# Kernel tuning notes

Measured on AMD Instinct MI355X. Metric: run time of the kernel, lower is better.

The kernel has to match this reference:

```python
import jax, jax.numpy as jnp
import numpy as np

NUM_CLASSES = 60
FEATURE_DIM = 256
SEQ_LEN = 128
NUM_HEADS = 8
TOP_M = 20  # min(20, seq_len)
NUM_LAYERS = 2
EPS = 1e-5


def _layernorm(x, g, b):
    m = x.mean(-1, keepdims=True)
    v = ((x - m) ** 2).mean(-1, keepdims=True)
    return (x - m) * jax.lax.rsqrt(v + EPS) * g + b


def _topm_attention(x, qkv_w, qkv_b, proj_w, proj_b):
    # x: (B, N, C). Weights stored as (in, out) so y = x @ W + b.
    B, N, C = x.shape
    hd = C // NUM_HEADS
    scale = hd ** -0.5
    qkv = (x @ qkv_w + qkv_b).reshape(B, N, 3, NUM_HEADS, hd)
    q, k, v = (jnp.moveaxis(qkv[:, :, i], 2, 1) for i in range(3))  # (B,H,N,hd)
    s = jnp.einsum('bhnd,bhmd->bhnm', q, k) * scale  # (B,H,N,N)
    if TOP_M < N:
        # keep only per-query top-m scores (threshold at the m-th largest;
        # identical to torch scatter-mask for distinct float scores)
        kth = jax.lax.top_k(s, TOP_M)[0][..., -1:]
        s = jnp.where(s >= kth, s, -jnp.inf)
    a = jax.nn.softmax(s, axis=-1)  # dropout is identity in eval
    o = jnp.einsum('bhnm,bhmd->bhnd', a, v)
    o = o.transpose(0, 2, 1, 3).reshape(B, N, C)
    return o @ proj_w + proj_b


def setup_inputs() -> dict:
    key = jax.random.key(0)
    ks = jax.random.split(key, 20)
    B = 8 * NUM_CLASSES
    C = FEATURE_DIM
    d = {
        'reweighted_features': jax.random.normal(ks[0], (B, C, SEQ_LEN), jnp.float32),
        'pos_embed': jax.random.normal(ks[1], (1, SEQ_LEN, C), jnp.float32) * 0.02,
        'cls_w1': jax.random.normal(ks[2], (C, C // 2), jnp.float32) / np.sqrt(C),
        'cls_b1': jnp.zeros((C // 2,), jnp.float32),
        'cls_w2': jax.random.normal(ks[3], (C // 2, 1), jnp.float32) / np.sqrt(C // 2),
        'cls_b2': jnp.zeros((1,), jnp.float32),
    }
    for i in range(NUM_LAYERS):
        d[f'qkv_w{i}'] = jax.random.normal(ks[4 + 4 * i], (C, 3 * C), jnp.float32) / np.sqrt(C)
        d[f'qkv_b{i}'] = jnp.zeros((3 * C,), jnp.float32)
        d[f'proj_w{i}'] = jax.random.normal(ks[5 + 4 * i], (C, C), jnp.float32) / np.sqrt(C)
        d[f'proj_b{i}'] = jnp.zeros((C,), jnp.float32)
        d[f'ln_g{i}'] = jnp.ones((C,), jnp.float32)
        d[f'ln_b{i}'] = jnp.zeros((C,), jnp.float32)
    return d


def reference(reweighted_features, pos_embed, cls_w1, cls_b1, cls_w2, cls_b2,
              qkv_w0, qkv_b0, proj_w0, proj_b0, ln_g0, ln_b0,
              qkv_w1, qkv_b1, proj_w1, proj_b1, ln_g1, ln_b1):
    B = reweighted_features.shape[0] // NUM_CLASSES
    x = reweighted_features.transpose(0, 2, 1)  # (B*cls, N, C)
    x = x + pos_embed
    layers = [(qkv_w0, qkv_b0, proj_w0, proj_b0, ln_g0, ln_b0),
              (qkv_w1, qkv_b1, proj_w1, proj_b1, ln_g1, ln_b1)]
    for qw, qb, pw, pb, g, b in layers:
        x = _layernorm(x + _topm_attention(x, qw, qb, pw, pb), g, b)
    x = x.mean(axis=1)  # (B*cls, C)
    x = x.reshape(B, NUM_CLASSES, FEATURE_DIM)
    h = jax.nn.relu(x @ cls_w1 + cls_b1)  # dropout identity in eval
    logits = (h @ cls_w2 + cls_b2).reshape(B, NUM_CLASSES)
    return logits
```

## Files before the change

### kernel.cpp

```cpp
#include <hip/hip_runtime.h>
#include <hip/hip_bf16.h>
#include <cmath>

#define NSEQ 480
#define SEQN 128
#define CDIM 256
#define NH 8
#define HD 32
#define TOPM 20

typedef float f32x4 __attribute__((ext_vector_type(4)));
typedef short bf16x8 __attribute__((ext_vector_type(8)));

__device__ __forceinline__ unsigned short bf16_rn(float x) {
    unsigned int u = __float_as_uint(x);
    unsigned int r = (u + 0x7FFFu + ((u >> 16) & 1u)) >> 16;
    return (unsigned short)r;
}
__device__ __forceinline__ float bf16f(unsigned short h) {
    return __uint_as_float(((unsigned int)h) << 16);
}
__device__ __forceinline__ unsigned int okey(float v) {
    unsigned int u = __float_as_uint(v);
    return (u >> 31) ? ~u : (u | 0x80000000u);
}
__device__ __forceinline__ float okey_inv(unsigned int k) {
    return __uint_as_float((k >> 31) ? (k & 0x7FFFFFFFu) : ~k);
}
__device__ __forceinline__ unsigned pk_bf16(float a, float b) {
    union { __hip_bfloat162 h; unsigned u; } cv;
    cv.h = __float22bfloat162_rn(make_float2(a, b));
    return cv.u;
}
__device__ __forceinline__ void unpack_bf16x8(uint4 u, float* o) {
    o[0] = bf16f((unsigned short)(u.x & 0xffffu)); o[1] = bf16f((unsigned short)(u.x >> 16));
    o[2] = bf16f((unsigned short)(u.y & 0xffffu)); o[3] = bf16f((unsigned short)(u.y >> 16));
    o[4] = bf16f((unsigned short)(u.z & 0xffffu)); o[5] = bf16f((unsigned short)(u.z >> 16));
    o[6] = bf16f((unsigned short)(u.w & 0xffffu)); o[7] = bf16f((unsigned short)(u.w >> 16));
}

__global__ __launch_bounds__(256) void prep_kernel(const float* __restrict__ RW,
                                                   const float* __restrict__ POS,
                                                   unsigned short* __restrict__ XH,
                                                   unsigned short* __restrict__ XL) {
    int b = blockIdx.x, n0 = blockIdx.y * 32, c0 = blockIdx.z * 32;
    __shared__ float tile[32][33];
    int tx = threadIdx.x & 31, ty = threadIdx.x >> 5;
#pragma unroll
    for (int jj = 0; jj < 4; ++jj) {
        int c = c0 + ty + 8 * jj;
        tile[ty + 8 * jj][tx] = RW[((size_t)b * CDIM + c) * SEQN + n0 + tx];
    }
    __syncthreads();
#pragma unroll
    for (int jj = 0; jj < 4; ++jj) {
        int n = n0 + ty + 8 * jj;
        int c = c0 + tx;
        float val = tile[tx][ty + 8 * jj] + POS[n * CDIM + c];
        unsigned short hi = bf16_rn(val);
        size_t idx = (size_t)b * SEQN * CDIM + n * CDIM + c;
        XH[idx] = hi;
        XL[idx] = bf16_rn(val - bf16f(hi));
    }
}

__global__ __launch_bounds__(256) void wsplit_kernel(const float* __restrict__ W,
                                                     unsigned short* __restrict__ WtHi,
                                                     unsigned short* __restrict__ WtLo,
                                                     int ncols) {
    int k0 = blockIdx.x * 32, j0 = blockIdx.y * 32;
    __shared__ float tile[32][33];
    int tx = threadIdx.x & 31, ty = threadIdx.x >> 5;
#pragma unroll
    for (int jj = 0; jj < 4; ++jj)
        tile[ty + 8 * jj][tx] = W[(size_t)(k0 + ty + 8 * jj) * ncols + j0 + tx];
    __syncthreads();
#pragma unroll
    for (int jj = 0; jj < 4; ++jj) {
        float v = tile[tx][ty + 8 * jj];
        unsigned short hi = bf16_rn(v);
        unsigned short lo = bf16_rn(v - bf16f(hi));
        size_t idx = (size_t)(j0 + ty + 8 * jj) * 256 + k0 + tx;
        WtHi[idx] = hi;
        WtLo[idx] = lo;
    }
}

__global__ __launch_bounds__(256, 4) void attn_kernel(
    const unsigned short* __restrict__ XHi, const unsigned short* __restrict__ XLo,
    unsigned short* __restrict__ OH, unsigned short* __restrict__ OL,
    const unsigned short* __restrict__ WtHi, const unsigned short* __restrict__ WtLo,
    const float* __restrict__ BIAS) {
    const int bid = blockIdx.x;
    const int h = (bid >> 3) & 7;
    const int b = ((bid >> 6) << 3) | (bid & 7);
    const float scale = 0.17677669529663687f;

    __shared__ unsigned short qh[SEQN * HD], ql[SEQN * HD];
    __shared__ unsigned short kh[SEQN * HD], kl[SEQN * HD];
    __shared__ unsigned short vh[HD * SEQN];

    const int tid = threadIdx.x;
    const int w = tid >> 6;
    const int l = tid & 63;
    const int l15 = l & 15;
    const int sct = l >> 4;
    const size_t xbase = (size_t)b * SEQN * CDIM;

    f32x4 acc[2][6];
#pragma unroll
    for (int mi = 0; mi < 2; ++mi)
#pragma unroll
        for (int ni = 0; ni < 6; ++ni) acc[mi][ni] = (f32x4){0.f, 0.f, 0.f, 0.f};

#pragma unroll 2
    for (int ks = 0; ks < 8; ++ks) {
        const int kb = ks * 32;
        bf16x8 ahi[2], alo[2];
#pragma unroll
        for (int mi = 0; mi < 2; ++mi) {
            int row = w * 32 + mi * 16 + l15;
            size_t off = xbase + row * CDIM + kb + sct * 8;
            ahi[mi] = *reinterpret_cast<const bf16x8*>(XHi + off);
            alo[mi] = *reinterpret_cast<const bf16x8*>(XLo + off);
        }
#pragma unroll
        for (int ni = 0; ni < 6; ++ni) {
            int j = ((ni >> 1) << 8) + h * HD + ((ni & 1) << 4) + l15;
            const int woff = j * 256 + kb + sct * 8;
            bf16x8 bh = *reinterpret_cast<const bf16x8*>(WtHi + woff);
            if (ni < 4) {
                bf16x8 bl = *reinterpret_cast<const bf16x8*>(WtLo + woff);
#pragma unroll
                for (int mi = 0; mi < 2; ++mi) {
                    acc[mi][ni] = __builtin_amdgcn_mfma_f32_16x16x32_bf16(ahi[mi], bh, acc[mi][ni], 0, 0, 0);
                    acc[mi][ni] = __builtin_amdgcn_mfma_f32_16x16x32_bf16(ahi[mi], bl, acc[mi][ni], 0, 0, 0);
                    acc[mi][ni] = __builtin_amdgcn_mfma_f32_16x16x32_bf16(alo[mi], bh, acc[mi][ni], 0, 0, 0);
                }
            } else {
#pragma unroll
                for (int mi = 0; mi < 2; ++mi)
                    acc[mi][ni] = __builtin_amdgcn_mfma_f32_16x16x32_bf16(ahi[mi], bh, acc[mi][ni], 0, 0, 0);
            }
        }
    }
#pragma unroll
    for (int ni = 0; ni < 6; ++ni) {
        const int sel = ni >> 1;
        const int dcol = ((ni & 1) << 4) + l15;
        const float bias = BIAS[(sel << 8) + h * HD + dcol];
#pragma unroll
        for (int mi = 0; mi < 2; ++mi) {
            const int tb = w * 32 + mi * 16 + sct * 4;
            if (sel == 2) {
                float v0 = acc[mi][ni][0] + bias, v1 = acc[mi][ni][1] + bias;
                float v2 = acc[mi][ni][2] + bias, v3 = acc[mi][ni][3] + bias;
                unsigned pA = pk_bf16(v0, v1), pB = pk_bf16(v2, v3);
                int c0i = tb ^ ((dcol & 7) << 3);
                *reinterpret_cast<uint2*>(&vh[dcol * SEQN + c0i]) = make_uint2(pA, pB);
            } else {
                unsigned short* ph = sel ? kh : qh;
                unsigned short* pl = sel ? kl : ql;
#pragma unroll
                for (int r = 0; r < 4; ++r) {
                    float v = acc[mi][ni][r] + bias;
                    if (sel == 0) v *= scale;
                    unsigned short hi = bf16_rn(v);
                    int token = tb + r;
                    int idx = token * HD + (dcol ^ (((token >> 1) & 3) << 3));
                    ph[idx] = hi;
                    pl[idx] = bf16_rn(v - bf16f(hi));
                }
            }
        }
    }
    __syncthreads();

    f32x4 sacc[8][2];
#pragma unroll
    for (int mi = 0; mi < 8; ++mi)
#pragma unroll
        for (int ni = 0; ni < 2; ++ni) sacc[mi][ni] = (f32x4){0.f, 0.f, 0.f, 0.f};

    bf16x8 qfh[2], qfl[2];
#pragma unroll
    for (int ni = 0; ni < 2; ++ni) {
        int qrow = w * 32 + (ni << 4) + l15;
        int off = qrow * HD + ((sct * 8) ^ (((qrow >> 1) & 3) << 3));
        qfh[ni] = *reinterpret_cast<const bf16x8*>(qh + off);
        qfl[ni] = *reinterpret_cast<const bf16x8*>(ql + off);
    }
#pragma unroll
    for (int mi = 0; mi < 8; ++mi) {
        int krow = (mi << 4) + l15;
        int off = krow * HD + ((sct * 8) ^ (((krow >> 1) & 3) << 3));
        bf16x8 kfh = *reinterpret_cast<const bf16x8*>(kh + off);
        bf16x8 kfl = *reinterpret_cast<const bf16x8*>(kl + off);
#pragma unroll
        for (int ni = 0; ni < 2; ++ni) {
            sacc[mi][ni] = __builtin_amdgcn_mfma_f32_16x16x32_bf16(kfh, qfh[ni], sacc[mi][ni], 0, 0, 0);
            sacc[mi][ni] = __builtin_amdgcn_mfma_f32_16x16x32_bf16(kfh, qfl[ni], sacc[mi][ni], 0, 0, 0);
            sacc[mi][ni] = __builtin_amdgcn_mfma_f32_16x16x32_bf16(kfl, qfh[ni], sacc[mi][ni], 0, 0, 0);
        }
    }
#pragma unroll
    for (int mi = 0; mi < 8; ++mi)
#pragma unroll
        for (int ni = 0; ni < 2; ++ni)
#pragma unroll
            for (int r = 0; r < 4; ++r)
                sacc[mi][ni][r] = __uint_as_float(okey(sacc[mi][ni][r]));

    unsigned int km0 = 0u, km1 = 0u;
#pragma unroll
    for (int mi = 0; mi < 8; ++mi)
#pragma unroll
        for (int r = 0; r < 4; ++r) {
            km0 = max(km0, __float_as_uint(sacc[mi][0][r]));
            km1 = max(km1, __float_as_uint(sacc[mi][1][r]));
        }
    km0 = max(km0, (unsigned int)__shfl_xor((int)km0, 16));
    km0 = max(km0, (unsigned int)__shfl_xor((int)km0, 32));
    km1 = max(km1, (unsigned int)__shfl_xor((int)km1, 16));
    km1 = max(km1, (unsigned int)__shfl_xor((int)km1, 32));
    float mx0 = okey_inv(km0), mx1 = okey_inv(km1);

    unsigned p0, p1;
    {
        unsigned lo0 = 0u, hi0 = km0 + 1u, lo1 = 0u, hi1 = km1 + 1u;
        unsigned th0 = km0, th1 = km1;
        int dn0 = 0, dn1 = 0;
#pragma unroll 1
        for (int it = 0; it < 34; ++it) {
            if (__all(dn0 & dn1)) break;
            unsigned mid0 = lo0 + ((hi0 - lo0) >> 1);
            unsigned mid1 = lo1 + ((hi1 - lo1) >> 1);
            int c0 = 0, c1 = 0;
#pragma unroll
            for (int mi = 0; mi < 8; ++mi)
#pragma unroll
                for (int r = 0; r < 4; ++r) {
                    c0 += (__float_as_uint(sacc[mi][0][r]) >= mid0) ? 1 : 0;
                    c1 += (__float_as_uint(sacc[mi][1][r]) >= mid1) ? 1 : 0;
                }
            int mpk = c0 | (c1 << 8);
            mpk += __shfl_xor(mpk, 16);
            mpk += __shfl_xor(mpk, 32);
            c0 = mpk & 255;
            c1 = mpk >> 8;
            if (!dn0) {
                if (c0 == TOPM) { th0 = mid0; dn0 = 1; }
                else if (hi0 - lo0 <= 1u) { th0 = lo0; dn0 = 1; }
                else if (c0 > TOPM) lo0 = mid0;
                else hi0 = mid0;
            }
            if (!dn1) {
                if (c1 == TOPM) { th1 = mid1; dn1 = 1; }
                else if (hi1 - lo1 <= 1u) { th1 = lo1; dn1 = 1; }
                else if (c1 > TOPM) lo1 = mid1;
                else hi1 = mid1;
            }
        }
        p0 = th0; p1 = th1;
    }

    float s0 = 0.f, s1 = 0.f;
#pragma unroll
    for (int mi = 0; mi < 8; ++mi)
#pragma unroll
        for (int r = 0; r < 4; ++r) {
            unsigned int u0 = __float_as_uint(sacc[mi][0][r]);
            unsigned int u1 = __float_as_uint(sacc[mi][1][r]);
            float e0 = (u0 >= p0) ? __expf(okey_inv(u0) - mx0) : 0.f;
            float e1 = (u1 >= p1) ? __expf(okey_inv(u1) - mx1) : 0.f;
            sacc[mi][0][r] = e0;
            sacc[mi][1][r] = e1;
            s0 += e0;
            s1 += e1;
        }
    s0 += __shfl_xor(s0, 16);
    s0 += __shfl_xor(s0, 32);
    s1 += __shfl_xor(s1, 16);
    s1 += __shfl_xor(s1, 32);
    float i0 = 1.f / s0, i1 = 1.f / s1;

    unsigned w16[8][2][2];
#pragma unroll
    for (int mi = 0; mi < 8; ++mi)
#pragma unroll
        for (int ni = 0; ni < 2; ++ni)
#pragma unroll
            for (int p = 0; p < 2; ++p)
                w16[mi][ni][p] = pk_bf16(sacc[mi][ni][2 * p], sacc[mi][ni][2 * p + 1]);

    f32x4 oacc[2][2];
#pragma unroll
    for (int mi = 0; mi < 2; ++mi)
#pragma unroll
        for (int ni = 0; ni < 2; ++ni) oacc[mi][ni] = (f32x4){0.f, 0.f, 0.f, 0.f};

#pragma unroll
    for (int k = 0; k < 4; ++k) {
        bf16x8 bvh[2];
#pragma unroll
        for (int nio = 0; nio < 2; ++nio) {
            int drow = (nio << 4) + l15;
            int off = drow * SEQN + ((k * 32 + sct * 8) ^ ((drow & 7) << 3));
            bvh[nio] = *reinterpret_cast<const bf16x8*>(vh + off);
        }
#pragma unroll
        for (int mio = 0; mio < 2; ++mio) {
            union { unsigned u[4]; bf16x8 v8; } aw;
#pragma unroll
            for (int j = 0; j < 4; ++j) {
                int src = l15 + ((sct & 1) << 5) + ((j >> 1) << 4);
                unsigned a0 = (unsigned)__shfl((int)w16[2 * k][mio][j & 1], src);
                unsigned a1 = (unsigned)__shfl((int)w16[2 * k + 1][mio][j & 1], src);
                aw.u[j] = (sct >= 2) ? a1 : a0;
            }
#pragma unroll
            for (int nio = 0; nio < 2; ++nio)
                oacc[mio][nio] = __builtin_amdgcn_mfma_f32_16x16x32_bf16(aw.v8, bvh[nio], oacc[mio][nio], 0, 0, 0);
        }
    }
    float invO[2][4];
#pragma unroll
    for (int mio = 0; mio < 2; ++mio)
#pragma unroll
        for (int r = 0; r < 4; ++r)
            invO[mio][r] = __shfl(mio ? i1 : i0, sct * 4 + r);
#pragma unroll
    for (int mio = 0; mio < 2; ++mio)
#pragma unroll
        for (int nio = 0; nio < 2; ++nio)
#pragma unroll
            for (int r = 0; r < 4; ++r) {
                int token = w * 32 + mio * 16 + sct * 4 + r;
                int d = (nio << 4) + l15;
                size_t idx = ((size_t)b * SEQN + token) * CDIM + h * HD + d;
                float v = oacc[mio][nio][r] * invO[mio][r];
                unsigned short hi = bf16_rn(v);
                OH[idx] = hi;
                OL[idx] = bf16_rn(v - bf16f(hi));
            }
}

__global__ __launch_bounds__(256, 4) void projln_kernel(
    const unsigned short* __restrict__ OHp, const unsigned short* __restrict__ OLp,
    unsigned short* __restrict__ XH, unsigned short* __restrict__ XL,
    const unsigned short* __restrict__ W2H, const unsigned short* __restrict__ W2L,
    const float* __restrict__ PB, const float* __restrict__ G,
    const float* __restrict__ BB) {
    const int b = blockIdx.x;
    const int t0 = blockIdx.y * 32;
    __shared__ float vals[32 * 289];
    __shared__ float part[8][32][2];

    const int tid = threadIdx.x;
    const int w = tid >> 6;
    const int l = tid & 63;
    const int l15 = l & 15;
    const int sct = l >> 4;

    f32x4 acc[2][4];
#pragma unroll
    for (int mi = 0; mi < 2; ++mi)
#pragma unroll
        for (int ni = 0; ni < 4; ++ni) acc[mi][ni] = (f32x4){0.f, 0.f, 0.f, 0.f};

    const size_t obase = ((size_t)b * SEQN + t0) * CDIM;
#pragma unroll 2
    for (int ks = 0; ks < 8; ++ks) {
        const int kb = ks * 32;
        bf16x8 ahi[2], alo[2];
#pragma unroll
        for (int mi = 0; mi < 2; ++mi) {
            size_t off = obase + (size_t)(mi * 16 + l15) * CDIM + kb + sct * 8;
            ahi[mi] = *reinterpret_cast<const bf16x8*>(OHp + off);
            alo[mi] = *reinterpret_cast<const bf16x8*>(OLp + off);
        }
#pragma unroll
        for (int ni = 0; ni < 4; ++ni) {
            int j = w * 64 + ni * 16 + l15;
            int woff = j * 256 + kb + sct * 8;
            bf16x8 bh = *reinterpret_cast<const bf16x8*>(W2H + woff);
            bf16x8 bl = *reinterpret_cast<const bf16x8*>(W2L + woff);
#pragma unroll
            for (int mi = 0; mi < 2; ++mi) {
                acc[mi][ni] = __builtin_amdgcn_mfma_f32_16x16x32_bf16(ahi[mi], bh, acc[mi][ni], 0, 0, 0);
                acc[mi][ni] = __builtin_amdgcn_mfma_f32_16x16x32_bf16(ahi[mi], bl, acc[mi][ni], 0, 0, 0);
                acc[mi][ni] = __builtin_amdgcn_mfma_f32_16x16x32_bf16(alo[mi], bh, acc[mi][ni], 0, 0, 0);
            }
        }
    }
#pragma unroll
    for (int ni = 0; ni < 4; ++ni) {
        int j = w * 64 + ni * 16 + l15;
        float bias = PB[j];
#pragma unroll
        for (int mi = 0; mi < 2; ++mi)
#pragma unroll
            for (int r = 0; r < 4; ++r) {
                int tok = mi * 16 + sct * 4 + r;
                vals[tok * 289 + j] = acc[mi][ni][r] + bias;
            }
    }
    __syncthreads();

    const int row = tid & 31;
    const int cc = tid >> 5;
    const size_t rbase = ((size_t)b * SEQN + t0 + row) * CDIM + cc * 32;
    float v[32];
    {
        float ps = 0.f, pq = 0.f;
#pragma unroll
        for (int q = 0; q < 4; ++q) {
            uint4 hb = *reinterpret_cast<const uint4*>(XH + rbase + q * 8);
            uint4 lb = *reinterpret_cast<const uint4*>(XL + rbase + q * 8);
            float rh[8], rl[8];
            unpack_bf16x8(hb, rh);
            unpack_bf16x8(lb, rl);
#pragma unroll
            for (int jj = 0; jj < 8; ++jj) {
                int col = cc * 32 + q * 8 + jj;
                float val = vals[row * 289 + col] + rh[jj] + rl[jj];
                v[q * 8 + jj] = val;
                ps += val;
                pq = fmaf(val, val, pq);
            }
        }
        part[cc][row][0] = ps;
        part[cc][row][1] = pq;
    }
    __syncthreads();
    float s1 = 0.f, s2 = 0.f;
#pragma unroll
    for (int k = 0; k < 8; ++k) { s1 += part[k][row][0]; s2 += part[k][row][1]; }
    float m = s1 * (1.f / 256.f);
    float var = s2 * (1.f / 256.f) - m * m;
    float rstd = rsqrtf(var + 1e-5f);
#pragma unroll
    for (int q = 0; q < 4; ++q) {
        int col0 = cc * 32 + q * 8;
        float4 g0 = *reinterpret_cast<const float4*>(G + col0);
        float4 g1 = *reinterpret_cast<const float4*>(G + col0 + 4);
        float4 b0 = *reinterpret_cast<const float4*>(BB + col0);
        float4 b1 = *reinterpret_cast<const float4*>(BB + col0 + 4);
        float gg[8] = {g0.x, g0.y, g0.z, g0.w, g1.x, g1.y, g1.z, g1.w};
        float bb2[8] = {b0.x, b0.y, b0.z, b0.w, b1.x, b1.y, b1.z, b1.w};
        unsigned hw[4], lw[4];
#pragma unroll
        for (int p2 = 0; p2 < 4; ++p2) {
            float y0 = (v[q * 8 + p2 * 2] - m) * rstd * gg[p2 * 2] + bb2[p2 * 2];
            float y1 = (v[q * 8 + p2 * 2 + 1] - m) * rstd * gg[p2 * 2 + 1] + bb2[p2 * 2 + 1];
            unsigned short h0 = bf16_rn(y0), h1 = bf16_rn(y1);
            unsigned short lo0 = bf16_rn(y0 - bf16f(h0)), lo1 = bf16_rn(y1 - bf16f(h1));
            hw[p2] = (unsigned)h0 | ((unsigned)h1 << 16);
            lw[p2] = (unsigned)lo0 | ((unsigned)lo1 << 16);
        }
        *reinterpret_cast<uint4*>(XH + rbase + q * 8) = make_uint4(hw[0], hw[1], hw[2], hw[3]);
        *reinterpret_cast<uint4*>(XL + rbase + q * 8) = make_uint4(lw[0], lw[1], lw[2], lw[3]);
    }
}

__global__ __launch_bounds__(256) void cls_kernel(const unsigned short* __restrict__ XH,
                                                  const unsigned short* __restrict__ XL,
                                                  const float* __restrict__ W1,
                                                  const float* __restrict__ B1,
                                                  const float* __restrict__ W2,
                                                  const float* __restrict__ B2,
                                                  float* __restrict__ OUT) {
    int b = blockIdx.x;
    __shared__ float xm[256];
    __shared__ float hred[128];
    int tid = threadIdx.x;
    float sm = 0.f;
    for (int n = 0; n < SEQN; ++n) {
        size_t idx = ((size_t)b * SEQN + n) * CDIM + tid;
        sm += bf16f(XH[idx]) + bf16f(XL[idx]);
    }
    xm[tid] = sm * (1.f / 128.f);
    __syncthreads();
    if (tid < 128) {
        float a = B1[tid];
        for (int k = 0; k < CDIM; ++k) a = fmaf(xm[k], W1[k * 128 + tid], a);
        a = fmaxf(a, 0.f);
        hred[tid] = a * W2[tid];
    }
    __syncthreads();
    for (int off = 64; off > 0; off >>= 1) {
        if (tid < off) hred[tid] += hred[tid + off];
        __syncthreads();
    }
    if (tid == 0) OUT[b] = hred[0] + B2[0];
}

extern "C" void kernel_launch(void* const* d_in, const int* in_sizes, int n_in,
                              void* d_out, int out_size, void* d_ws, size_t ws_size,
                              hipStream_t stream) {
    const float* RW  = (const float*)d_in[0];
    const float* POS = (const float*)d_in[1];
    const float* CW1 = (const float*)d_in[2];
    const float* CB1 = (const float*)d_in[3];
    const float* CW2 = (const float*)d_in[4];
    const float* CB2 = (const float*)d_in[5];

    const size_t NTOK = (size_t)NSEQ * SEQN * CDIM;
    unsigned short* OH = (unsigned short*)d_ws;
    unsigned short* OL = OH + NTOK;
    unsigned short* XH = OL + NTOK;
    unsigned short* XL = XH + NTOK;
    unsigned short* WtHi = XL + NTOK;
    unsigned short* WtLo = WtHi + (size_t)768 * 256;
    unsigned short* W2H = WtLo + (size_t)768 * 256;
    unsigned short* W2L = W2H + (size_t)256 * 256;

    prep_kernel<<<dim3(NSEQ, 4, 8), 256, 0, stream>>>(RW, POS, XH, XL);

    for (int li = 0; li < 2; ++li) {
        const float* qw = (const float*)d_in[6 + 6 * li];
        const float* qb = (const float*)d_in[7 + 6 * li];
        const float* pw = (const float*)d_in[8 + 6 * li];
        const float* pb = (const float*)d_in[9 + 6 * li];
        const float* lg = (const float*)d_in[10 + 6 * li];
        const float* lb = (const float*)d_in[11 + 6 * li];
        wsplit_kernel<<<dim3(8, 24), 256, 0, stream>>>(qw, WtHi, WtLo, 768);
        wsplit_kernel<<<dim3(8, 8), 256, 0, stream>>>(pw, W2H, W2L, 256);
        attn_kernel<<<NSEQ * NH, 256, 0, stream>>>(XH, XL, OH, OL, WtHi, WtLo, qb);
        projln_kernel<<<dim3(NSEQ, 4), 256, 0, stream>>>(OH, OL, XH, XL, W2H, W2L, pb, lg, lb);
    }

    cls_kernel<<<NSEQ, 256, 0, stream>>>(XH, XL, CW1, CB1, CW2, CB2, (float*)d_out);
}
```

Before: 787.8 us.

## Split attention work across 8 waves and merge weight-split launches

The attention kernel now runs 512 threads (8 waves), each owning 16 query rows instead of 32, which halves per-wave accumulator registers and raises wave-level parallelism per block. MFMA sections are wrapped with s_setprio to favour matrix issue, and the two weight-splitting launches are merged into one kernel. The cost is duplicated weight-fragment loads across more waves and higher register-pressure limits from launch_bounds(512,8), which could cause spills.

```diff
diff --git a/kernel.cpp b/kernel.cpp
--- a/kernel.cpp
+++ b/kernel.cpp
@@ -64,11 +64,17 @@
     }
 }
 
-__global__ __launch_bounds__(256) void wsplit_kernel(const float* __restrict__ W,
-                                                     unsigned short* __restrict__ WtHi,
-                                                     unsigned short* __restrict__ WtLo,
-                                                     int ncols) {
-    int k0 = blockIdx.x * 32, j0 = blockIdx.y * 32;
+__global__ __launch_bounds__(256) void wsplit2_kernel(
+    const float* __restrict__ Wq, const float* __restrict__ Wp,
+    unsigned short* __restrict__ QH, unsigned short* __restrict__ QL,
+    unsigned short* __restrict__ PH, unsigned short* __restrict__ PL) {
+    int k0 = blockIdx.x * 32;
+    int yy = blockIdx.y;
+    const float* W;
+    unsigned short *WH, *WL;
+    int ncols, j0;
+    if (yy < 24) { W = Wq; WH = QH; WL = QL; ncols = 768; j0 = yy * 32; }
+    else         { W = Wp; WH = PH; WL = PL; ncols = 256; j0 = (yy - 24) * 32; }
     __shared__ float tile[32][33];
     int tx = threadIdx.x & 31, ty = threadIdx.x >> 5;
 #pragma unroll
@@ -81,12 +87,12 @@
         unsigned short hi = bf16_rn(v);
         unsigned short lo = bf16_rn(v - bf16f(hi));
         size_t idx = (size_t)(j0 + ty + 8 * jj) * 256 + k0 + tx;
-        WtHi[idx] = hi;
-        WtLo[idx] = lo;
-    }
-}
-
-__global__ __launch_bounds__(256, 4) void attn_kernel(
+        WH[idx] = hi;
+        WL[idx] = lo;
+    }
+}
+
+__global__ __launch_bounds__(512, 8) void attn_kernel(
     const unsigned short* __restrict__ XHi, const unsigned short* __restrict__ XLo,
     unsigned short* __restrict__ OH, unsigned short* __restrict__ OL,
     const unsigned short* __restrict__ WtHi, const unsigned short* __restrict__ WtLo,
@@ -107,23 +113,17 @@
     const int sct = l >> 4;
     const size_t xbase = (size_t)b * SEQN * CDIM;
 
-    f32x4 acc[2][6];
-#pragma unroll
-    for (int mi = 0; mi < 2; ++mi)
-#pragma unroll
-        for (int ni = 0; ni < 6; ++ni) acc[mi][ni] = (f32x4){0.f, 0.f, 0.f, 0.f};
+    f32x4 acc[6];
+#pragma unroll
+    for (int ni = 0; ni < 6; ++ni) acc[ni] = (f32x4){0.f, 0.f, 0.f, 0.f};
 
 #pragma unroll 2
     for (int ks = 0; ks < 8; ++ks) {
         const int kb = ks * 32;
-        bf16x8 ahi[2], alo[2];
-#pragma unroll
-        for (int mi = 0; mi < 2; ++mi) {
-            int row = w * 32 + mi * 16 + l15;
-            size_t off = xbase + row * CDIM + kb + sct * 8;
-            ahi[mi] = *reinterpret_cast<const bf16x8*>(XHi + off);
-            alo[mi] = *reinterpret_cast<const bf16x8*>(XLo + off);
-        }
+        const int row = w * 16 + l15;
+        size_t off = xbase + row * CDIM + kb + sct * 8;
+        bf16x8 ahi = *reinterpret_cast<const bf16x8*>(XHi + off);
+        bf16x8 alo = *reinterpret_cast<const bf16x8*>(XLo + off);
 #pragma unroll
         for (int ni = 0; ni < 6; ++ni) {
             int j = ((ni >> 1) << 8) + h * HD + ((ni & 1) << 4) + l15;
@@ -131,16 +131,11 @@
             bf16x8 bh = *reinterpret_cast<const bf16x8*>(WtHi + woff);
             if (ni < 4) {
                 bf16x8 bl = *reinterpret_cast<const bf16x8*>(WtLo + woff);
-#pragma unroll
-                for (int mi = 0; mi < 2; ++mi) {
-                    acc[mi][ni] = __builtin_amdgcn_mfma_f32_16x16x32_bf16(ahi[mi], bh, acc[mi][ni], 0, 0, 0);
-                    acc[mi][ni] = __builtin_amdgcn_mfma_f32_16x16x32_bf16(ahi[mi], bl, acc[mi][ni], 0, 0, 0);
-                    acc[mi][ni] = __builtin_amdgcn_mfma_f32_16x16x32_bf16(alo[mi], bh, acc[mi][ni], 0, 0, 0);
-                }
+                acc[ni] = __builtin_amdgcn_mfma_f32_16x16x32_bf16(ahi, bh, acc[ni], 0, 0, 0);
+                acc[ni] = __builtin_amdgcn_mfma_f32_16x16x32_bf16(ahi, bl, acc[ni], 0, 0, 0);
+                acc[ni] = __builtin_amdgcn_mfma_f32_16x16x32_bf16(alo, bh, acc[ni], 0, 0, 0);
             } else {
-#pragma unroll
-                for (int mi = 0; mi < 2; ++mi)
-                    acc[mi][ni] = __builtin_amdgcn_mfma_f32_16x16x32_bf16(ahi[mi], bh, acc[mi][ni], 0, 0, 0);
+                acc[ni] = __builtin_amdgcn_mfma_f32_16x16x32_bf16(ahi, bh, acc[ni], 0, 0, 0);
             }
         }
     }
@@ -149,155 +144,115 @@
         const int sel = ni >> 1;
         const int dcol = ((ni & 1) << 4) + l15;
         const float bias = BIAS[(sel << 8) + h * HD + dcol];
-#pragma unroll
-        for (int mi = 0; mi < 2; ++mi) {
-            const int tb = w * 32 + mi * 16 + sct * 4;
-            if (sel == 2) {
-                float v0 = acc[mi][ni][0] + bias, v1 = acc[mi][ni][1] + bias;
-                float v2 = acc[mi][ni][2] + bias, v3 = acc[mi][ni][3] + bias;
-                unsigned pA = pk_bf16(v0, v1), pB = pk_bf16(v2, v3);
-                int c0i = tb ^ ((dcol & 7) << 3);
-                *reinterpret_cast<uint2*>(&vh[dcol * SEQN + c0i]) = make_uint2(pA, pB);
-            } else {
-                unsigned short* ph = sel ? kh : qh;
-                unsigned short* pl = sel ? kl : ql;
-#pragma unroll
-                for (int r = 0; r < 4; ++r) {
-                    float v = acc[mi][ni][r] + bias;
-                    if (sel == 0) v *= scale;
-                    unsigned short hi = bf16_rn(v);
-                    int token = tb + r;
-                    int idx = token * HD + (dcol ^ (((token >> 1) & 3) << 3));
-                    ph[idx] = hi;
-                    pl[idx] = bf16_rn(v - bf16f(hi));
-                }
-            }
-        }
-    }
-    __syncthreads();
-
-    f32x4 sacc[8][2];
-#pragma unroll
-    for (int mi = 0; mi < 8; ++mi)
-#pragma unroll
-        for (int ni = 0; ni < 2; ++ni) sacc[mi][ni] = (f32x4){0.f, 0.f, 0.f, 0.f};
-
-    bf16x8 qfh[2], qfl[2];
-#pragma unroll
-    for (int ni = 0; ni < 2; ++ni) {
-        int qrow = w * 32 + (ni << 4) + l15;
-        int off = qrow * HD + ((sct * 8) ^ (((qrow >> 1) & 3) << 3));
-        qfh[ni] = *reinterpret_cast<const bf16x8*>(qh + off);
-        qfl[ni] = *reinterpret_cast<const bf16x8*>(ql + off);
-    }
+        const int tb = w * 16 + sct * 4;
+        if (sel == 2) {
+            float v0 = acc[ni][0] + bias, v1 = acc[ni][1] + bias;
+            float v2 = acc[ni][2] + bias, v3 = acc[ni][3] + bias;
+            unsigned pA = pk_bf16(v0, v1), pB = pk_bf16(v2, v3);
+            int c0i = tb ^ ((dcol & 7) << 3);
+            *reinterpret_cast<uint2*>(&vh[dcol * SEQN + c0i]) = make_uint2(pA, pB);
+        } else {
+            unsigned short* ph = sel ? kh : qh;
+            unsigned short* pl = sel ? kl : ql;
+#pragma unroll
+            for (int r = 0; r < 4; ++r) {
+                float v = acc[ni][r] + bias;
+                if (sel == 0) v *= scale;
+                unsigned short hi = bf16_rn(v);
+                int token = tb + r;
+                int idx = token * HD + (dcol ^ (((token >> 1) & 3) << 3));
+                ph[idx] = hi;
+                pl[idx] = bf16_rn(v - bf16f(hi));
+            }
+        }
+    }
+    __syncthreads();
+
+    f32x4 sacc[8];
+#pragma unroll
+    for (int mi = 0; mi < 8; ++mi) sacc[mi] = (f32x4){0.f, 0.f, 0.f, 0.f};
+
+    const int qrow = w * 16 + l15;
+    const int qoff = qrow * HD + ((sct * 8) ^ (((qrow >> 1) & 3) << 3));
+    bf16x8 qfh = *reinterpret_cast<const bf16x8*>(qh + qoff);
+    bf16x8 qfl = *reinterpret_cast<const bf16x8*>(ql + qoff);
+    __builtin_amdgcn_s_setprio(1);
 #pragma unroll
     for (int mi = 0; mi < 8; ++mi) {
         int krow = (mi << 4) + l15;
         int off = krow * HD + ((sct * 8) ^ (((krow >> 1) & 3) << 3));
         bf16x8 kfh = *reinterpret_cast<const bf16x8*>(kh + off);
         bf16x8 kfl = *reinterpret_cast<const bf16x8*>(kl + off);
-#pragma unroll
-        for (int ni = 0; ni < 2; ++ni) {
-            sacc[mi][ni] = __builtin_amdgcn_mfma_f32_16x16x32_bf16(kfh, qfh[ni], sacc[mi][ni], 0, 0, 0);
-            sacc[mi][ni] = __builtin_amdgcn_mfma_f32_16x16x32_bf16(kfh, qfl[ni], sacc[mi][ni], 0, 0, 0);
-            sacc[mi][ni] = __builtin_amdgcn_mfma_f32_16x16x32_bf16(kfl, qfh[ni], sacc[mi][ni], 0, 0, 0);
-        }
-    }
+        sacc[mi] = __builtin_amdgcn_mfma_f32_16x16x32_bf16(kfh, qfh, sacc[mi], 0, 0, 0);
+        sacc[mi] = __builtin_amdgcn_mfma_f32_16x16x32_bf16(kfh, qfl, sacc[mi], 0, 0, 0);
+        sacc[mi] = __builtin_amdgcn_mfma_f32_16x16x32_bf16(kfl, qfh, sacc[mi], 0, 0, 0);
+    }
+    __builtin_amdgcn_s_setprio(0);
 #pragma unroll
     for (int mi = 0; mi < 8; ++mi)
 #pragma unroll
-        for (int ni = 0; ni < 2; ++ni)
-#pragma unroll
-            for (int r = 0; r < 4; ++r)
-                sacc[mi][ni][r] = __uint_as_float(okey(sacc[mi][ni][r]));
-
-    unsigned int km0 = 0u, km1 = 0u;
+        for (int r = 0; r < 4; ++r)
+            sacc[mi][r] = __uint_as_float(okey(sacc[mi][r]));
+
+    unsigned int km = 0u;
 #pragma unroll
     for (int mi = 0; mi < 8; ++mi)
 #pragma unroll
-        for (int r = 0; r < 4; ++r) {
-            km0 = max(km0, __float_as_uint(sacc[mi][0][r]));
-            km1 = max(km1, __float_as_uint(sacc[mi][1][r]));
-        }
-    km0 = max(km0, (unsigned int)__shfl_xor((int)km0, 16));
-    km0 = max(km0, (unsigned int)__shfl_xor((int)km0, 32));
-    km1 = max(km1, (unsigned int)__shfl_xor((int)km1, 16));
-    km1 = max(km1, (unsigned int)__shfl_xor((int)km1, 32));
-    float mx0 = okey_inv(km0), mx1 = okey_inv(km1);
-
-    unsigned p0, p1;
+        for (int r = 0; r < 4; ++r) km = max(km, __float_as_uint(sacc[mi][r]));
+    km = max(km, (unsigned int)__shfl_xor((int)km, 16));
+    km = max(km, (unsigned int)__shfl_xor((int)km, 32));
+    float mx = okey_inv(km);
+
+    unsigned p0;
     {
-        unsigned lo0 = 0u, hi0 = km0 + 1u, lo1 = 0u, hi1 = km1 + 1u;
-        unsigned th0 = km0, th1 = km1;
-        int dn0 = 0, dn1 = 0;
+        unsigned lo = 0u, hi = km + 1u, th = km;
+        int dn = 0;
 #pragma unroll 1
         for (int it = 0; it < 34; ++it) {
-            if (__all(dn0 & dn1)) break;
-            unsigned mid0 = lo0 + ((hi0 - lo0) >> 1);
-            unsigned mid1 = lo1 + ((hi1 - lo1) >> 1);
-            int c0 = 0, c1 = 0;
+            if (__all(dn)) break;
+            unsigned mid = lo + ((hi - lo) >> 1);
+            int c = 0;
 #pragma unroll
             for (int mi = 0; mi < 8; ++mi)
 #pragma unroll
-                for (int r = 0; r < 4; ++r) {
-                    c0 += (__float_as_uint(sacc[mi][0][r]) >= mid0) ? 1 : 0;
-                    c1 += (__float_as_uint(sacc[mi][1][r]) >= mid1) ? 1 : 0;
-                }
-            int mpk = c0 | (c1 << 8);
-            mpk += __shfl_xor(mpk, 16);
-            mpk += __shfl_xor(mpk, 32);
-            c0 = mpk & 255;
-            c1 = mpk >> 8;
-            if (!dn0) {
-                if (c0 == TOPM) { th0 = mid0; dn0 = 1; }
-                else if (hi0 - lo0 <= 1u) { th0 = lo0; dn0 = 1; }
-                else if (c0 > TOPM) lo0 = mid0;
-                else hi0 = mid0;
-            }
-            if (!dn1) {
-                if (c1 == TOPM) { th1 = mid1; dn1 = 1; }
-                else if (hi1 - lo1 <= 1u) { th1 = lo1; dn1 = 1; }
-                else if (c1 > TOPM) lo1 = mid1;
-                else hi1 = mid1;
-            }
-        }
-        p0 = th0; p1 = th1;
-    }
-
-    float s0 = 0.f, s1 = 0.f;
+                for (int r = 0; r < 4; ++r)
+                    c += (__float_as_uint(sacc[mi][r]) >= mid) ? 1 : 0;
+            c += __shfl_xor(c, 16);
+            c += __shfl_xor(c, 32);
+            if (!dn) {
+                if (c == TOPM) { th = mid; dn = 1; }
+                else if (hi - lo <= 1u) { th = lo; dn = 1; }
+                else if (c > TOPM) lo = mid;
+                else hi = mid;
+            }
+        }
+        p0 = th;
+    }
+
+    float s0 = 0.f;
 #pragma unroll
     for (int mi = 0; mi < 8; ++mi)
 #pragma unroll
         for (int r = 0; r < 4; ++r) {
-            unsigned int u0 = __float_as_uint(sacc[mi][0][r]);
-            unsigned int u1 = __float_as_uint(sacc[mi][1][r]);
-            float e0 = (u0 >= p0) ? __expf(okey_inv(u0) - mx0) : 0.f;
-            float e1 = (u1 >= p1) ? __expf(okey_inv(u1) - mx1) : 0.f;
-            sacc[mi][0][r] = e0;
-            sacc[mi][1][r] = e1;
+            unsigned int u0 = __float_as_uint(sacc[mi][r]);
+            float e0 = (u0 >= p0) ? __expf(okey_inv(u0) - mx) : 0.f;
+            sacc[mi][r] = e0;
             s0 += e0;
-            s1 += e1;
         }
     s0 += __shfl_xor(s0, 16);
     s0 += __shfl_xor(s0, 32);
-    s1 += __shfl_xor(s1, 16);
-    s1 += __shfl_xor(s1, 32);
-    float i0 = 1.f / s0, i1 = 1.f / s1;
-
-    unsigned w16[8][2][2];
+    float i0 = 1.f / s0;
+
+    unsigned w16a[8][2];
 #pragma unroll
     for (int mi = 0; mi < 8; ++mi)
 #pragma unroll
-        for (int ni = 0; ni < 2; ++ni)
-#pragma unroll
-            for (int p = 0; p < 2; ++p)
-                w16[mi][ni][p] = pk_bf16(sacc[mi][ni][2 * p], sacc[mi][ni][2 * p + 1]);
-
-    f32x4 oacc[2][2];
-#pragma unroll
-    for (int mi = 0; mi < 2; ++mi)
-#pragma unroll
-        for (int ni = 0; ni < 2; ++ni) oacc[mi][ni] = (f32x4){0.f, 0.f, 0.f, 0.f};
+        for (int p = 0; p < 2; ++p)
+            w16a[mi][p] = pk_bf16(sacc[mi][2 * p], sacc[mi][2 * p + 1]);
+
+    f32x4 oacc[2];
+#pragma unroll
+    for (int ni = 0; ni < 2; ++ni) oacc[ni] = (f32x4){0.f, 0.f, 0.f, 0.f};
 
 #pragma unroll
     for (int k = 0; k < 4; ++k) {
@@ -308,41 +263,35 @@
             int off = drow * SEQN + ((k * 32 + sct * 8) ^ ((drow & 7) << 3));
             bvh[nio] = *reinterpret_cast<const bf16x8*>(vh + off);
         }
-#pragma unroll
-        for (int mio = 0; mio < 2; ++mio) {
-            union { unsigned u[4]; bf16x8 v8; } aw;
-#pragma unroll
-            for (int j = 0; j < 4; ++j) {
-                int src = l15 + ((sct & 1) << 5) + ((j >> 1) << 4);
-                unsigned a0 = (unsigned)__shfl((int)w16[2 * k][mio][j & 1], src);
-                unsigned a1 = (unsigned)__shfl((int)w16[2 * k + 1][mio][j & 1], src);
-                aw.u[j] = (sct >= 2) ? a1 : a0;
-            }
-#pragma unroll
-            for (int nio = 0; nio < 2; ++nio)
-                oacc[mio][nio] = __builtin_amdgcn_mfma_f32_16x16x32_bf16(aw.v8, bvh[nio], oacc[mio][nio], 0, 0, 0);
-        }
-    }
-    float invO[2][4];
-#pragma unroll
-    for (int mio = 0; mio < 2; ++mio)
-#pragma unroll
-        for (int r = 0; r < 4; ++r)
-            invO[mio][r] = __shfl(mio ? i1 : i0, sct * 4 + r);
-#pragma unroll
-    for (int mio = 0; mio < 2; ++mio)
+        union { unsigned u[4]; bf16x8 v8; } aw;
+#pragma unroll
+        for (int j = 0; j < 4; ++j) {
+            int src = l15 + ((sct & 1) << 5) + ((j >> 1) << 4);
+            unsigned a0 = (unsigned)__shfl((int)w16a[2 * k][j & 1], src);
+            unsigned a1 = (unsigned)__shfl((int)w16a[2 * k + 1][j & 1], src);
+            aw.u[j] = (sct >= 2) ? a1 : a0;
+        }
+        __builtin_amdgcn_s_setprio(1);
 #pragma unroll
         for (int nio = 0; nio < 2; ++nio)
-#pragma unroll
-            for (int r = 0; r < 4; ++r) {
-                int token = w * 32 + mio * 16 + sct * 4 + r;
-                int d = (nio << 4) + l15;
-                size_t idx = ((size_t)b * SEQN + token) * CDIM + h * HD + d;
-                float v = oacc[mio][nio][r] * invO[mio][r];
-                unsigned short hi = bf16_rn(v);
-                OH[idx] = hi;
-                OL[idx] = bf16_rn(v - bf16f(hi));
-            }
+            oacc[nio] = __builtin_amdgcn_mfma_f32_16x16x32_bf16(aw.v8, bvh[nio], oacc[nio], 0, 0, 0);
+        __builtin_amdgcn_s_setprio(0);
+    }
+    float invO[4];
+#pragma unroll
+    for (int r = 0; r < 4; ++r) invO[r] = __shfl(i0, sct * 4 + r);
+#pragma unroll
+    for (int nio = 0; nio < 2; ++nio)
+#pragma unroll
+        for (int r = 0; r < 4; ++r) {
+            int token = w * 16 + sct * 4 + r;
+            int d = (nio << 4) + l15;
+            size_t idx = ((size_t)b * SEQN + token) * CDIM + h * HD + d;
+            float v = oacc[nio][r] * invO[r];
+            unsigned short hi = bf16_rn(v);
+            OH[idx] = hi;
+            OL[idx] = bf16_rn(v - bf16f(hi));
+        }
 }
 
 __global__ __launch_bounds__(256, 4) void projln_kernel(
@@ -524,9 +473,8 @@
         const float* pb = (const float*)d_in[9 + 6 * li];
         const float* lg = (const float*)d_in[10 + 6 * li];
         const float* lb = (const float*)d_in[11 + 6 * li];
-        wsplit_kernel<<<dim3(8, 24), 256, 0, stream>>>(qw, WtHi, WtLo, 768);
-        wsplit_kernel<<<dim3(8, 8), 256, 0, stream>>>(pw, W2H, W2L, 256);
-        attn_kernel<<<NSEQ * NH, 256, 0, stream>>>(XH, XL, OH, OL, WtHi, WtLo, qb);
+        wsplit2_kernel<<<dim3(8, 32), 256, 0, stream>>>(qw, pw, WtHi, WtLo, W2H, W2L);
+        attn_kernel<<<NSEQ * NH, 512, 0, stream>>>(XH, XL, OH, OL, WtHi, WtLo, qb);
         projln_kernel<<<dim3(NSEQ, 4), 256, 0, stream>>>(OH, OL, XH, XL, W2H, W2L, pb, lg, lb);
     }
 
```

Measured after the change: 1.186 ms. +50.6%, slower.
